# Kernel tuning notes

Measured on AMD Instinct MI355X. Metric: run time of the kernel, lower is better.

## Reference

```python
import jax, jax.numpy as jnp
import numpy as np

N_NODES = 50000
N_EDGES = 800000
IN_CH = 128
OUT_CH = 64  # hidden = 2*OUT_CH = 128


def setup_inputs() -> dict:
    key = jax.random.key(0)
    ks = jax.random.split(key, 5)
    x = jax.random.normal(ks[0], (N_NODES, IN_CH), dtype=jnp.float32)
    edge_index = jax.random.randint(ks[1], (2, N_EDGES), 0, N_NODES, dtype=jnp.int32)
    # Glorot-ish scaled weights for the two GCNConv layers
    W1 = jax.random.normal(ks[2], (IN_CH, 2 * OUT_CH), dtype=jnp.float32) * 0.05
    b1 = jnp.zeros((2 * OUT_CH,), dtype=jnp.float32)
    W2 = jax.random.normal(ks[3], (2 * OUT_CH, OUT_CH), dtype=jnp.float32) * 0.05
    b2 = jnp.zeros((OUT_CH,), dtype=jnp.float32)
    return {"x": x, "edge_index": edge_index, "W1": W1, "b1": b1, "W2": W2, "b2": b2}


def reference(x, edge_index, W1, b1, W2, b2):
    N = x.shape[0]
    # GCN normalization with self-loops (PyG GCNConv default):
    # A_hat = A + I, deg from target nodes, norm = d_i^-1/2 * d_j^-1/2
    loops = jnp.arange(N, dtype=edge_index.dtype)
    row = jnp.concatenate([edge_index[0], loops])  # source
    col = jnp.concatenate([edge_index[1], loops])  # target
    deg = jax.ops.segment_sum(jnp.ones(row.shape, x.dtype), col, num_segments=N)
    dinv = jnp.where(deg > 0, jax.lax.rsqrt(deg), 0.0)
    norm = dinv[row] * dinv[col]  # [E+N]

    def conv(h, W, b):
        h = h @ W                           # [N, D_out] transform first (D_out <= D_in path)
        msg = norm[:, None] * h[row]        # gather + scale: [E+N, D_out]
        agg = jax.ops.segment_sum(msg, col, num_segments=N)
        return agg + b

    h = jax.nn.relu(conv(x, W1, b1))
    return conv(h, W2, b2)
```

## Files before the change

### kernel.cpp

```cpp
#include <hip/hip_runtime.h>
#include <hip/hip_bf16.h>
#include <hip/hip_fp16.h>

#define IN_CH  128
#define HID    128
#define OUTC   64

#define NSCAT 256
#define SLOTC 64
#define CAPB  6144
#define CAP2  6144
#define TSTRIDE 140

typedef _Float16 half8 __attribute__((ext_vector_type(8)));
typedef _Float16 half4v __attribute__((ext_vector_type(4)));
typedef float float4v __attribute__((ext_vector_type(4)));

__device__ __forceinline__ void vacc(float4v& a0, float4v& a1, half8 u) {
    half4v lo = __builtin_shufflevector(u, u, 0, 1, 2, 3);
    half4v hi = __builtin_shufflevector(u, u, 4, 5, 6, 7);
    a0 += __builtin_convertvector(lo, float4v);
    a1 += __builtin_convertvector(hi, float4v);
}
__device__ __forceinline__ void vaccw(float4v& a0, float4v& a1, half8 u, float w) {
    half4v lo = __builtin_shufflevector(u, u, 0, 1, 2, 3);
    half4v hi = __builtin_shufflevector(u, u, 4, 5, 6, 7);
    a0 += w * __builtin_convertvector(lo, float4v);
    a1 += w * __builtin_convertvector(hi, float4v);
}

__global__ __launch_bounds__(256) void scatA_kernel(
        const int* __restrict__ src, const int* __restrict__ dst,
        unsigned* __restrict__ tmp2, ushort* __restrict__ cnts,
        const float* __restrict__ W1, const float* __restrict__ W2,
        _Float16* __restrict__ Wt1, _Float16* __restrict__ Wt2,
        int E, int N, int NBK, int chunk) {
    __shared__ int cnt[256];
    int t = threadIdx.x, blk = blockIdx.x;
    cnt[t] = 0;
    __syncthreads();
    int base = blk * chunk;
    int end = base + chunk; if (end > E) end = E;
    for (int e = base + t; e < end; e += 256) {
        unsigned d = (unsigned)dst[e];
        unsigned s = (unsigned)src[e];
        int b = d >> 8;
        int pos = atomicAdd(&cnt[b], 1);
        if (pos < SLOTC)
            tmp2[((size_t)(b << 8) + blk) * SLOTC + pos] = (d << 16) | s;
    }
    __syncthreads();
    if (t < NBK) {
        int c = cnt[t]; if (c > SLOTC) c = SLOTC;
        cnts[t * 256 + blk] = (ushort)c;
    }

    for (int idx = blk * 256 + t; idx < 128 * 128 + 128 * 64; idx += NSCAT * 256) {
        if (idx < 128 * 128) {
            int k = idx >> 7, nn = idx & 127;
            Wt1[nn * 128 + k] = (_Float16)W1[idx];
        } else {
            int j = idx - 128 * 128;
            int k = j >> 6, nn = j & 63;
            Wt2[nn * 128 + k] = (_Float16)W2[j];
        }
    }
}

__global__ __launch_bounds__(256) void csrB_kernel(
        const unsigned* __restrict__ tmp2, const ushort* __restrict__ cnts,
        int* __restrict__ off, ushort* __restrict__ degs, float* __restrict__ dinv,
        ushort* __restrict__ srcs,
        const float* __restrict__ x, _Float16* __restrict__ xh,
        int N, int NBK) {
    __shared__ int ex[257];
    __shared__ int h[256], cur[256];
    __shared__ unsigned ein[CAP2];
    __shared__ ushort outb[CAP2];
    __shared__ float dsh[256];
    int b = blockIdx.x, t = threadIdx.x;

    int c = cnts[b * 256 + t];
    h[t] = c;
    __syncthreads();
    for (int d = 1; d < 256; d <<= 1) {
        int v = (t >= d) ? h[t - d] : 0;
        __syncthreads();
        h[t] += v;
        __syncthreads();
    }
    ex[t] = h[t] - c;
    if (t == 255) ex[256] = h[255];
    __syncthreads();
    int total = ex[256]; if (total > CAP2) total = CAP2;

    for (int i = t; i < total; i += 256) {
        int lo = 0, hi = 255;
        while (lo < hi) {
            int mid = (lo + hi + 1) >> 1;
            if (ex[mid] <= i) lo = mid; else hi = mid - 1;
        }
        ein[i] = tmp2[((size_t)(b << 8) + lo) * SLOTC + (i - ex[lo])];
    }
    __syncthreads();

    h[t] = 0;
    __syncthreads();
    for (int i = t; i < total; i += 256)
        atomicAdd(&h[(ein[i] >> 16) & 255], 1);
    __syncthreads();
    int cdeg = h[t];
    for (int d = 1; d < 256; d <<= 1) {
        int v = (t >= d) ? h[t - d] : 0;
        __syncthreads();
        h[t] += v;
        __syncthreads();
    }
    int excl = h[t] - cdeg;
    int node = (b << 8) + t;
    float dv = rsqrtf((float)(cdeg + 1));
    if (node < N) {
        off[node] = b * CAPB + excl;
        degs[node] = (ushort)cdeg;
        dinv[node] = dv;
    }
    dsh[t] = (node < N) ? dv : 0.f;
    cur[t] = excl;
    __syncthreads();
    for (int i = t; i < total; i += 256) {
        unsigned v = ein[i];
        int pos = atomicAdd(&cur[(v >> 16) & 255], 1);
        outb[pos] = (ushort)(v & 0xFFFFu);
    }
    __syncthreads();
    for (int i = t; i < total; i += 256) srcs[b * CAPB + i] = outb[i];

    int rowbase = b << 8;
    for (int m = t; m < 256 * 16; m += 256) {
        int r = m >> 4, k = m & 15;
        int nd = rowbase + r;
        if (nd < N) {
            const float4* xp = (const float4*)(x + (size_t)nd * 128 + k * 8);
            float4 v0 = xp[0], v1 = xp[1];
            float di = dsh[r];
            half8 o = { (_Float16)(di * v0.x), (_Float16)(di * v0.y),
                        (_Float16)(di * v0.z), (_Float16)(di * v0.w),
                        (_Float16)(di * v1.x), (_Float16)(di * v1.y),
                        (_Float16)(di * v1.z), (_Float16)(di * v1.w) };
            ((half8*)xh)[(size_t)nd * 16 + k] = o;
        }
    }
}

__global__ __launch_bounds__(256, 8) void agg1_kernel(const _Float16* __restrict__ xh,
                                                      const int* __restrict__ off,
                                                      const ushort* __restrict__ degs,
                                                      const ushort* __restrict__ srcs,
                                                      const float* __restrict__ dinv,
                                                      _Float16* __restrict__ A1, int N) {
    int grp = threadIdx.x >> 4;
    int p   = threadIdx.x & 15;
    int node = blockIdx.x * 16 + grp;
    if (node >= N) return;
    int s = off[node];
    int e = s + degs[node];

    const half8* xs = (const half8*)xh;
    float4v a0 = (float4v)0.f, a1 = (float4v)0.f;
    float4v c0 = (float4v)0.f, c1 = (float4v)0.f;

    int j = s;
    for (; j + 8 <= e; j += 8) {
        int i0 = srcs[j], i1 = srcs[j+1], i2 = srcs[j+2], i3 = srcs[j+3];
        int i4 = srcs[j+4], i5 = srcs[j+5], i6 = srcs[j+6], i7 = srcs[j+7];
        half8 u0 = xs[(size_t)i0 * 16 + p];
        half8 u1 = xs[(size_t)i1 * 16 + p];
        half8 u2 = xs[(size_t)i2 * 16 + p];
        half8 u3 = xs[(size_t)i3 * 16 + p];
        half8 u4 = xs[(size_t)i4 * 16 + p];
        half8 u5 = xs[(size_t)i5 * 16 + p];
        half8 u6 = xs[(size_t)i6 * 16 + p];
        half8 u7 = xs[(size_t)i7 * 16 + p];
        vacc(a0, a1, u0); vacc(c0, c1, u1);
        vacc(a0, a1, u2); vacc(c0, c1, u3);
        vacc(a0, a1, u4); vacc(c0, c1, u5);
        vacc(a0, a1, u6); vacc(c0, c1, u7);
    }
    if (j + 4 <= e) {
        int i0 = srcs[j], i1 = srcs[j+1], i2 = srcs[j+2], i3 = srcs[j+3];
        half8 u0 = xs[(size_t)i0 * 16 + p];
        half8 u1 = xs[(size_t)i1 * 16 + p];
        half8 u2 = xs[(size_t)i2 * 16 + p];
        half8 u3 = xs[(size_t)i3 * 16 + p];
        vacc(a0, a1, u0); vacc(c0, c1, u1);
        vacc(a0, a1, u2); vacc(c0, c1, u3);
        j += 4;
    }
    int rm = e - j;
    if (rm > 0) {
        int i0 = srcs[j];
        int i1 = srcs[rm > 1 ? j + 1 : j];
        int i2 = srcs[rm > 2 ? j + 2 : j];
        float w1 = (rm > 1) ? 1.f : 0.f;
        float w2 = (rm > 2) ? 1.f : 0.f;
        half8 u0 = xs[(size_t)i0 * 16 + p];
        half8 u1 = xs[(size_t)i1 * 16 + p];
        half8 u2 = xs[(size_t)i2 * 16 + p];
        vacc(a0, a1, u0);
        vaccw(c0, c1, u1, w1);
        vaccw(c0, c1, u2, w2);
    }
    a0 += c0; a1 += c1;

    float di = dinv[node];
    half8 sv = xs[(size_t)node * 16 + p];
    half4v slo = __builtin_shufflevector(sv, sv, 0, 1, 2, 3);
    half4v shi = __builtin_shufflevector(sv, sv, 4, 5, 6, 7);
    a0 += __builtin_convertvector(slo, float4v);
    a1 += __builtin_convertvector(shi, float4v);
    a0 *= di; a1 *= di;
    half4v h0 = __builtin_convertvector(a0, half4v);
    half4v h1 = __builtin_convertvector(a1, half4v);
    half8 hh = __builtin_shufflevector(h0, h1, 0, 1, 2, 3, 4, 5, 6, 7);
    *((half8*)(A1 + (size_t)node * 128) + p) = hh;
}

__global__ __launch_bounds__(256) void gemm_fused_kernel(
        const _Float16* __restrict__ A1, const _Float16* __restrict__ Wt1,
        const float* __restrict__ b1, const _Float16* __restrict__ Wt2,
        const float* __restrict__ dinv, _Float16* __restrict__ H3s, int N) {
    __shared__ _Float16 tile[4][32 * TSTRIDE];
    int wave = threadIdx.x >> 6;
    int lane = threadIdx.x & 63;
    int n16 = lane & 15;
    int q   = lane >> 4;
    int rowBase = blockIdx.x * 128 + wave * 32;

    half8 a[2][4];
#pragma unroll
    for (int rt = 0; rt < 2; ++rt) {
        int row = rowBase + rt * 16 + n16;
        if (row >= N) row = N - 1;
        const _Float16* ap = A1 + (size_t)row * 128 + q * 8;
#pragma unroll
        for (int kb = 0; kb < 4; ++kb)
            a[rt][kb] = *(const half8*)(ap + kb * 32);
    }

    float4v acc1[2][8];
#pragma unroll
    for (int rt = 0; rt < 2; ++rt)
#pragma unroll
        for (int ct = 0; ct < 8; ++ct) acc1[rt][ct] = (float4v)0.f;
#pragma unroll
    for (int ct = 0; ct < 8; ++ct) {
        const _Float16* bp = Wt1 + (size_t)(ct * 16 + n16) * 128 + q * 8;
        half8 b[4];
#pragma unroll
        for (int kb = 0; kb < 4; ++kb) b[kb] = *(const half8*)(bp + kb * 32);
#pragma unroll
        for (int kb = 0; kb < 4; ++kb) {
            acc1[0][ct] = __builtin_amdgcn_mfma_f32_16x16x32_f16(a[0][kb], b[kb], acc1[0][ct], 0, 0, 0);
            acc1[1][ct] = __builtin_amdgcn_mfma_f32_16x16x32_f16(a[1][kb], b[kb], acc1[1][ct], 0, 0, 0);
        }
    }

    _Float16* tw = &tile[wave][0];
#pragma unroll
    for (int ct = 0; ct < 8; ++ct) {
        int col = ct * 16 + n16;
        float bv = b1[col];
#pragma unroll
        for (int rt = 0; rt < 2; ++rt)
#pragma unroll
            for (int r = 0; r < 4; ++r) {
                int row = rt * 16 + q * 4 + r;
                tw[row * TSTRIDE + col] = (_Float16)fmaxf(acc1[rt][ct][r] + bv, 0.f);
            }
    }
    __syncthreads();

    half8 a2[2][4];
#pragma unroll
    for (int rt = 0; rt < 2; ++rt) {
        const _Float16* tp = tw + (rt * 16 + n16) * TSTRIDE + q * 8;
#pragma unroll
        for (int kb = 0; kb < 4; ++kb)
            a2[rt][kb] = *(const half8*)(tp + kb * 32);
    }

    float4v acc2[2][4];
#pragma unroll
    for (int rt = 0; rt < 2; ++rt)
#pragma unroll
        for (int ct = 0; ct < 4; ++ct) acc2[rt][ct] = (float4v)0.f;
#pragma unroll
    for (int ct = 0; ct < 4; ++ct) {
        const _Float16* bp = Wt2 + (size_t)(ct * 16 + n16) * 128 + q * 8;
        half8 b[4];
#pragma unroll
        for (int kb = 0; kb < 4; ++kb) b[kb] = *(const half8*)(bp + kb * 32);
#pragma unroll
        for (int kb = 0; kb < 4; ++kb) {
            acc2[0][ct] = __builtin_amdgcn_mfma_f32_16x16x32_f16(a2[0][kb], b[kb], acc2[0][ct], 0, 0, 0);
            acc2[1][ct] = __builtin_amdgcn_mfma_f32_16x16x32_f16(a2[1][kb], b[kb], acc2[1][ct], 0, 0, 0);
        }
    }

#pragma unroll
    for (int rt = 0; rt < 2; ++rt)
#pragma unroll
        for (int ct = 0; ct < 4; ++ct) {
            int col = ct * 16 + n16;
#pragma unroll
            for (int r = 0; r < 4; ++r) {
                int row = rowBase + rt * 16 + q * 4 + r;
                if (row < N)
                    H3s[(size_t)row * OUTC + col] = (_Float16)(acc2[rt][ct][r] * dinv[row]);
            }
        }
}

__global__ __launch_bounds__(256, 8) void agg2_kernel(const _Float16* __restrict__ H3s,
                                                      const int* __restrict__ off,
                                                      const ushort* __restrict__ degs,
                                                      const ushort* __restrict__ srcs,
                                                      const float* __restrict__ dinv,
                                                      const float* __restrict__ bias,
                                                      float* __restrict__ out, int N) {
    int grp = threadIdx.x >> 3;
    int p   = threadIdx.x & 7;
    int node = blockIdx.x * 32 + grp;
    if (node >= N) return;
    int s = off[node];
    int e = s + degs[node];

    const half8* hs = (const half8*)H3s;
    float4v a0 = (float4v)0.f, a1 = (float4v)0.f;
    float4v c0 = (float4v)0.f, c1 = (float4v)0.f;

    int j = s;
    for (; j + 8 <= e; j += 8) {
        int i0 = srcs[j], i1 = srcs[j+1], i2 = srcs[j+2], i3 = srcs[j+3];
        int i4 = srcs[j+4], i5 = srcs[j+5], i6 = srcs[j+6], i7 = srcs[j+7];
        half8 u0 = hs[(size_t)i0 * 8 + p];
        half8 u1 = hs[(size_t)i1 * 8 + p];
        half8 u2 = hs[(size_t)i2 * 8 + p];
        half8 u3 = hs[(size_t)i3 * 8 + p];
        half8 u4 = hs[(size_t)i4 * 8 + p];
        half8 u5 = hs[(size_t)i5 * 8 + p];
        half8 u6 = hs[(size_t)i6 * 8 + p];
        half8 u7 = hs[(size_t)i7 * 8 + p];
        vacc(a0, a1, u0); vacc(c0, c1, u1);
        vacc(a0, a1, u2); vacc(c0, c1, u3);
        vacc(a0, a1, u4); vacc(c0, c1, u5);
        vacc(a0, a1, u6); vacc(c0, c1, u7);
    }
    if (j + 4 <= e) {
        int i0 = srcs[j], i1 = srcs[j+1], i2 = srcs[j+2], i3 = srcs[j+3];
        half8 u0 = hs[(size_t)i0 * 8 + p];
        half8 u1 = hs[(size_t)i1 * 8 + p];
        half8 u2 = hs[(size_t)i2 * 8 + p];
        half8 u3 = hs[(size_t)i3 * 8 + p];
        vacc(a0, a1, u0); vacc(c0, c1, u1);
        vacc(a0, a1, u2); vacc(c0, c1, u3);
        j += 4;
    }
    int rm = e - j;
    if (rm > 0) {
        int i0 = srcs[j];
        int i1 = srcs[rm > 1 ? j + 1 : j];
        int i2 = srcs[rm > 2 ? j + 2 : j];
        float w1 = (rm > 1) ? 1.f : 0.f;
        float w2 = (rm > 2) ? 1.f : 0.f;
        half8 u0 = hs[(size_t)i0 * 8 + p];
        half8 u1 = hs[(size_t)i1 * 8 + p];
        half8 u2 = hs[(size_t)i2 * 8 + p];
        vacc(a0, a1, u0);
        vaccw(c0, c1, u1, w1);
        vaccw(c0, c1, u2, w2);
    }
    a0 += c0; a1 += c1;

    float di = dinv[node];
    half8 sv = hs[(size_t)node * 8 + p];
    half4v slo = __builtin_shufflevector(sv, sv, 0, 1, 2, 3);
    half4v shi = __builtin_shufflevector(sv, sv, 4, 5, 6, 7);
    a0 += __builtin_convertvector(slo, float4v);
    a1 += __builtin_convertvector(shi, float4v);
    const float4v* bp = (const float4v*)(bias + p * 8);
    float4v o0 = di * a0 + bp[0];
    float4v o1 = di * a1 + bp[1];
    float4v* op = (float4v*)(out + (size_t)node * 64 + p * 8);
    op[0] = o0; op[1] = o1;
}

extern "C" void kernel_launch(void* const* d_in, const int* in_sizes, int n_in,
                              void* d_out, int out_size, void* d_ws, size_t ws_size,
                              hipStream_t stream) {
    const float* x   = (const float*)d_in[0];
    const int*   ei  = (const int*)d_in[1];
    const float* W1  = (const float*)d_in[2];
    const float* b1  = (const float*)d_in[3];
    const float* W2  = (const float*)d_in[4];
    const float* b2  = (const float*)d_in[5];
    float* out = (float*)d_out;

    const int N = in_sizes[0] / IN_CH;
    const int E = in_sizes[1] / 2;
    const int* src = ei;
    const int* dst = ei + E;

    const int NBK = (N + 255) >> 8;
    const int chunk = (E + NSCAT - 1) / NSCAT;

    auto align256 = [](size_t v) { return (v + 255) & ~(size_t)255; };
    char* w = (char*)d_ws;
    int* off = (int*)w;              w += align256((size_t)N * 4);
    ushort* degs = (ushort*)w;       w += align256((size_t)N * 2);
    float* dinv = (float*)w;         w += align256((size_t)N * 4);
    ushort* cnts = (ushort*)w;       w += align256((size_t)NBK * 256 * 2);
    ushort* srcs = (ushort*)w;       w += align256((size_t)NBK * CAPB * 2);
    _Float16* Wt1 = (_Float16*)w;    w += align256((size_t)HID * 128 * 2);
    _Float16* Wt2 = (_Float16*)w;    w += align256((size_t)OUTC * 128 * 2);
    size_t reg1 = align256((size_t)NBK * 256 * SLOTC * 4);
    if (reg1 < align256((size_t)N * HID * 2)) reg1 = align256((size_t)N * HID * 2);
    unsigned* tmp2 = (unsigned*)w;
    _Float16* A1 = (_Float16*)w;     w += reg1;
    _Float16* xh = (_Float16*)w;
    _Float16* H3s = (_Float16*)w;    w += align256((size_t)N * HID * 2);

    scatA_kernel<<<NSCAT, 256, 0, stream>>>(src, dst, tmp2, cnts,
                                            W1, W2, Wt1, Wt2, E, N, NBK, chunk);
    csrB_kernel<<<NBK, 256, 0, stream>>>(tmp2, cnts, off, degs, dinv, srcs,
                                         x, xh, N, NBK);

    agg1_kernel<<<(N + 15) / 16, 256, 0, stream>>>(xh, off, degs, srcs, dinv, A1, N);
    gemm_fused_kernel<<<(N + 127) / 128, 256, 0, stream>>>(A1, Wt1, b1, Wt2, dinv, H3s, N);
    agg2_kernel<<<(N + 31) / 32, 256, 0, stream>>>(H3s, off, degs, srcs, dinv, b2, out, N);
}
```

Before: 181.3 us.

## Pad CSR neighbor lists to multiples of eight with self-index, vectorize index loads

The CSR build now pads each node's neighbor list to a multiple of eight by filling the extra slots with the node's own index. Both aggregation kernels can then drop their tail handling, read indices as 16-byte vectors, and subtract the padded self-contributions through a weighted self-term. The edge scatter loads src/dst as int4 with a grid-stride loop, and the csrB prefix sums switch to wavefront shuffle scans. Bucket capacity grows to hold the padding, which raises LDS use and adds redundant gathers for the padded slots.

```diff
diff --git a/kernel.cpp b/kernel.cpp
--- a/kernel.cpp
+++ b/kernel.cpp
@@ -8,8 +8,8 @@
 
 #define NSCAT 256
 #define SLOTC 64
-#define CAPB  6144
-#define CAP2  6144
+#define CAPB  7168
+#define CAP2  7168
 #define TSTRIDE 140
 
 typedef _Float16 half8 __attribute__((ext_vector_type(8)));
@@ -34,16 +34,43 @@
         unsigned* __restrict__ tmp2, ushort* __restrict__ cnts,
         const float* __restrict__ W1, const float* __restrict__ W2,
         _Float16* __restrict__ Wt1, _Float16* __restrict__ Wt2,
-        int E, int N, int NBK, int chunk) {
+        int E, int N, int NBK) {
     __shared__ int cnt[256];
     int t = threadIdx.x, blk = blockIdx.x;
     cnt[t] = 0;
     __syncthreads();
-    int base = blk * chunk;
-    int end = base + chunk; if (end > E) end = E;
-    for (int e = base + t; e < end; e += 256) {
-        unsigned d = (unsigned)dst[e];
-        unsigned s = (unsigned)src[e];
+    int E4 = E >> 2;
+    for (int q = blk * 256 + t; q < E4; q += NSCAT * 256) {
+        int4 s4 = ((const int4*)src)[q];
+        int4 d4 = ((const int4*)dst)[q];
+        {
+            int b = ((unsigned)d4.x) >> 8;
+            int pos = atomicAdd(&cnt[b], 1);
+            if (pos < SLOTC)
+                tmp2[((size_t)(b << 8) + blk) * SLOTC + pos] = (((unsigned)d4.x) << 16) | (unsigned)s4.x;
+        }
+        {
+            int b = ((unsigned)d4.y) >> 8;
+            int pos = atomicAdd(&cnt[b], 1);
+            if (pos < SLOTC)
+                tmp2[((size_t)(b << 8) + blk) * SLOTC + pos] = (((unsigned)d4.y) << 16) | (unsigned)s4.y;
+        }
+        {
+            int b = ((unsigned)d4.z) >> 8;
+            int pos = atomicAdd(&cnt[b], 1);
+            if (pos < SLOTC)
+                tmp2[((size_t)(b << 8) + blk) * SLOTC + pos] = (((unsigned)d4.z) << 16) | (unsigned)s4.z;
+        }
+        {
+            int b = ((unsigned)d4.w) >> 8;
+            int pos = atomicAdd(&cnt[b], 1);
+            if (pos < SLOTC)
+                tmp2[((size_t)(b << 8) + blk) * SLOTC + pos] = (((unsigned)d4.w) << 16) | (unsigned)s4.w;
+        }
+    }
+    if (blk == 0 && t < (E & 3)) {
+        int e = (E4 << 2) + t;
+        unsigned d = (unsigned)dst[e], s = (unsigned)src[e];
         int b = d >> 8;
         int pos = atomicAdd(&cnt[b], 1);
         if (pos < SLOTC)
@@ -74,23 +101,30 @@
         const float* __restrict__ x, _Float16* __restrict__ xh,
         int N, int NBK) {
     __shared__ int ex[257];
-    __shared__ int h[256], cur[256];
+    __shared__ int hcnt[256], cur[256];
     __shared__ unsigned ein[CAP2];
     __shared__ ushort outb[CAP2];
     __shared__ float dsh[256];
+    __shared__ int wsum[4], wsum2[4], atot_s;
     int b = blockIdx.x, t = threadIdx.x;
+    int lane = t & 63, wid = t >> 6;
 
     int c = cnts[b * 256 + t];
-    h[t] = c;
-    __syncthreads();
-    for (int d = 1; d < 256; d <<= 1) {
-        int v = (t >= d) ? h[t - d] : 0;
-        __syncthreads();
-        h[t] += v;
-        __syncthreads();
-    }
-    ex[t] = h[t] - c;
-    if (t == 255) ex[256] = h[255];
+    int x1 = c;
+#pragma unroll
+    for (int d = 1; d < 64; d <<= 1) {
+        int y = __shfl_up(x1, d, 64);
+        if (lane >= d) x1 += y;
+    }
+    if (lane == 63) wsum[wid] = x1;
+    __syncthreads();
+    {
+        int add = 0;
+        for (int k = 0; k < wid; ++k) add += wsum[k];
+        x1 += add;
+    }
+    ex[t] = x1 - c;
+    if (t == 255) ex[256] = x1;
     __syncthreads();
     int total = ex[256]; if (total > CAP2) total = CAP2;
 
@@ -104,19 +138,30 @@
     }
     __syncthreads();
 
-    h[t] = 0;
+    hcnt[t] = 0;
     __syncthreads();
     for (int i = t; i < total; i += 256)
-        atomicAdd(&h[(ein[i] >> 16) & 255], 1);
-    __syncthreads();
-    int cdeg = h[t];
-    for (int d = 1; d < 256; d <<= 1) {
-        int v = (t >= d) ? h[t - d] : 0;
-        __syncthreads();
-        h[t] += v;
-        __syncthreads();
-    }
-    int excl = h[t] - cdeg;
+        atomicAdd(&hcnt[(ein[i] >> 16) & 255], 1);
+    __syncthreads();
+    int cdeg = hcnt[t];
+    int adeg = (cdeg + 7) & ~7;
+
+    int x2 = adeg;
+#pragma unroll
+    for (int d = 1; d < 64; d <<= 1) {
+        int y = __shfl_up(x2, d, 64);
+        if (lane >= d) x2 += y;
+    }
+    if (lane == 63) wsum2[wid] = x2;
+    __syncthreads();
+    {
+        int add = 0;
+        for (int k = 0; k < wid; ++k) add += wsum2[k];
+        x2 += add;
+    }
+    int excl = x2 - adeg;
+    if (t == 255) atot_s = x2;
+
     int node = (b << 8) + t;
     float dv = rsqrtf((float)(cdeg + 1));
     if (node < N) {
@@ -133,7 +178,10 @@
         outb[pos] = (ushort)(v & 0xFFFFu);
     }
     __syncthreads();
-    for (int i = t; i < total; i += 256) srcs[b * CAPB + i] = outb[i];
+    for (int k = excl + cdeg; k < excl + adeg; ++k) outb[k] = (ushort)node;
+    __syncthreads();
+    int atot = atot_s;
+    for (int i = t; i < atot; i += 256) srcs[b * CAPB + i] = outb[i];
 
     int rowbase = b << 8;
     for (int m = t; m < 256 * 16; m += 256) {
@@ -163,16 +211,22 @@
     int node = blockIdx.x * 16 + grp;
     if (node >= N) return;
     int s = off[node];
-    int e = s + degs[node];
+    int deg = degs[node];
+    int adeg = (deg + 7) & ~7;
+    int pcnt = adeg - deg;
 
     const half8* xs = (const half8*)xh;
     float4v a0 = (float4v)0.f, a1 = (float4v)0.f;
     float4v c0 = (float4v)0.f, c1 = (float4v)0.f;
 
-    int j = s;
-    for (; j + 8 <= e; j += 8) {
-        int i0 = srcs[j], i1 = srcs[j+1], i2 = srcs[j+2], i3 = srcs[j+3];
-        int i4 = srcs[j+4], i5 = srcs[j+5], i6 = srcs[j+6], i7 = srcs[j+7];
+    const uint4* sp = (const uint4*)(srcs + s);
+    int nr = adeg >> 3;
+    for (int r = 0; r < nr; ++r) {
+        uint4 iv = sp[r];
+        int i0 = iv.x & 0xFFFF, i1 = iv.x >> 16;
+        int i2 = iv.y & 0xFFFF, i3 = iv.y >> 16;
+        int i4 = iv.z & 0xFFFF, i5 = iv.z >> 16;
+        int i6 = iv.w & 0xFFFF, i7 = iv.w >> 16;
         half8 u0 = xs[(size_t)i0 * 16 + p];
         half8 u1 = xs[(size_t)i1 * 16 + p];
         half8 u2 = xs[(size_t)i2 * 16 + p];
@@ -186,38 +240,11 @@
         vacc(a0, a1, u4); vacc(c0, c1, u5);
         vacc(a0, a1, u6); vacc(c0, c1, u7);
     }
-    if (j + 4 <= e) {
-        int i0 = srcs[j], i1 = srcs[j+1], i2 = srcs[j+2], i3 = srcs[j+3];
-        half8 u0 = xs[(size_t)i0 * 16 + p];
-        half8 u1 = xs[(size_t)i1 * 16 + p];
-        half8 u2 = xs[(size_t)i2 * 16 + p];
-        half8 u3 = xs[(size_t)i3 * 16 + p];
-        vacc(a0, a1, u0); vacc(c0, c1, u1);
-        vacc(a0, a1, u2); vacc(c0, c1, u3);
-        j += 4;
-    }
-    int rm = e - j;
-    if (rm > 0) {
-        int i0 = srcs[j];
-        int i1 = srcs[rm > 1 ? j + 1 : j];
-        int i2 = srcs[rm > 2 ? j + 2 : j];
-        float w1 = (rm > 1) ? 1.f : 0.f;
-        float w2 = (rm > 2) ? 1.f : 0.f;
-        half8 u0 = xs[(size_t)i0 * 16 + p];
-        half8 u1 = xs[(size_t)i1 * 16 + p];
-        half8 u2 = xs[(size_t)i2 * 16 + p];
-        vacc(a0, a1, u0);
-        vaccw(c0, c1, u1, w1);
-        vaccw(c0, c1, u2, w2);
-    }
     a0 += c0; a1 += c1;
 
     float di = dinv[node];
     half8 sv = xs[(size_t)node * 16 + p];
-    half4v slo = __builtin_shufflevector(sv, sv, 0, 1, 2, 3);
-    half4v shi = __builtin_shufflevector(sv, sv, 4, 5, 6, 7);
-    a0 += __builtin_convertvector(slo, float4v);
-    a1 += __builtin_convertvector(shi, float4v);
+    vaccw(a0, a1, sv, (float)(1 - pcnt));
     a0 *= di; a1 *= di;
     half4v h0 = __builtin_convertvector(a0, half4v);
     half4v h1 = __builtin_convertvector(a1, half4v);
@@ -333,16 +360,22 @@
     int node = blockIdx.x * 32 + grp;
     if (node >= N) return;
     int s = off[node];
-    int e = s + degs[node];
+    int deg = degs[node];
+    int adeg = (deg + 7) & ~7;
+    int pcnt = adeg - deg;
 
     const half8* hs = (const half8*)H3s;
     float4v a0 = (float4v)0.f, a1 = (float4v)0.f;
     float4v c0 = (float4v)0.f, c1 = (float4v)0.f;
 
-    int j = s;
-    for (; j + 8 <= e; j += 8) {
-        int i0 = srcs[j], i1 = srcs[j+1], i2 = srcs[j+2], i3 = srcs[j+3];
-        int i4 = srcs[j+4], i5 = srcs[j+5], i6 = srcs[j+6], i7 = srcs[j+7];
+    const uint4* sp = (const uint4*)(srcs + s);
+    int nr = adeg >> 3;
+    for (int r = 0; r < nr; ++r) {
+        uint4 iv = sp[r];
+        int i0 = iv.x & 0xFFFF, i1 = iv.x >> 16;
+        int i2 = iv.y & 0xFFFF, i3 = iv.y >> 16;
+        int i4 = iv.z & 0xFFFF, i5 = iv.z >> 16;
+        int i6 = iv.w & 0xFFFF, i7 = iv.w >> 16;
         half8 u0 = hs[(size_t)i0 * 8 + p];
         half8 u1 = hs[(size_t)i1 * 8 + p];
         half8 u2 = hs[(size_t)i2 * 8 + p];
@@ -356,38 +389,11 @@
         vacc(a0, a1, u4); vacc(c0, c1, u5);
         vacc(a0, a1, u6); vacc(c0, c1, u7);
     }
-    if (j + 4 <= e) {
-        int i0 = srcs[j], i1 = srcs[j+1], i2 = srcs[j+2], i3 = srcs[j+3];
-        half8 u0 = hs[(size_t)i0 * 8 + p];
-        half8 u1 = hs[(size_t)i1 * 8 + p];
-        half8 u2 = hs[(size_t)i2 * 8 + p];
-        half8 u3 = hs[(size_t)i3 * 8 + p];
-        vacc(a0, a1, u0); vacc(c0, c1, u1);
-        vacc(a0, a1, u2); vacc(c0, c1, u3);
-        j += 4;
-    }
-    int rm = e - j;
-    if (rm > 0) {
-        int i0 = srcs[j];
-        int i1 = srcs[rm > 1 ? j + 1 : j];
-        int i2 = srcs[rm > 2 ? j + 2 : j];
-        float w1 = (rm > 1) ? 1.f : 0.f;
-        float w2 = (rm > 2) ? 1.f : 0.f;
-        half8 u0 = hs[(size_t)i0 * 8 + p];
-        half8 u1 = hs[(size_t)i1 * 8 + p];
-        half8 u2 = hs[(size_t)i2 * 8 + p];
-        vacc(a0, a1, u0);
-        vaccw(c0, c1, u1, w1);
-        vaccw(c0, c1, u2, w2);
-    }
     a0 += c0; a1 += c1;
 
     float di = dinv[node];
     half8 sv = hs[(size_t)node * 8 + p];
-    half4v slo = __builtin_shufflevector(sv, sv, 0, 1, 2, 3);
-    half4v shi = __builtin_shufflevector(sv, sv, 4, 5, 6, 7);
-    a0 += __builtin_convertvector(slo, float4v);
-    a1 += __builtin_convertvector(shi, float4v);
+    vaccw(a0, a1, sv, (float)(1 - pcnt));
     const float4v* bp = (const float4v*)(bias + p * 8);
     float4v o0 = di * a0 + bp[0];
     float4v o1 = di * a1 + bp[1];
@@ -412,7 +418,6 @@
     const int* dst = ei + E;
 
     const int NBK = (N + 255) >> 8;
-    const int chunk = (E + NSCAT - 1) / NSCAT;
 
     auto align256 = [](size_t v) { return (v + 255) & ~(size_t)255; };
     char* w = (char*)d_ws;
@@ -431,7 +436,7 @@
     _Float16* H3s = (_Float16*)w;    w += align256((size_t)N * HID * 2);
 
     scatA_kernel<<<NSCAT, 256, 0, stream>>>(src, dst, tmp2, cnts,
-                                            W1, W2, Wt1, Wt2, E, N, NBK, chunk);
+                                            W1, W2, Wt1, Wt2, E, N, NBK);
     csrB_kernel<<<NBK, 256, 0, stream>>>(tmp2, cnts, off, degs, dinv, srcs,
                                          x, xh, N, NBK);
 
```

New measurement: 178.1 us, median of 2. Within noise of the previous version (-1.7%).
